# Performance work log

Hardware: AMD Instinct MI355X
Metric: run time of the kernel (lower is better)

The kernel has to match this reference:

```python
import jax, jax.numpy as jnp
import numpy as np

NHID = 512
T_K, T_Q, B = 256, 128, 8


def setup_inputs() -> dict:
    key = jax.random.key(0)
    k1, k2, k3, k4, k5 = jax.random.split(key, 5)
    query = jax.random.normal(k1, (T_Q, B, NHID), dtype=jnp.float32)
    c_key = jax.random.normal(k2, (T_K, B, NHID), dtype=jnp.float32)
    mask = jax.random.randint(k3, (T_K, B), 0, 2).astype(bool)
    # att_mlp params: Linear(2*nhid, nhid) -> Tanh -> Linear(nhid, 1)
    # stored as [in, out] so y = x @ W + b (torch Linear weight transposed)
    W1 = jax.random.normal(k4, (2 * NHID, NHID), dtype=jnp.float32) / np.sqrt(2 * NHID)
    b1 = jnp.zeros((NHID,), dtype=jnp.float32)
    W2 = jax.random.normal(k5, (NHID, 1), dtype=jnp.float32) / np.sqrt(NHID)
    b2 = jnp.zeros((1,), dtype=jnp.float32)
    return {"query": query, "c_key": c_key, "mask": mask,
            "W1": W1, "b1": b1, "W2": W2, "b2": b2}


def reference(query, c_key, mask, W1, b1, W2, b2):
    H = query.shape[-1]
    # cat([k_expand, q_expand], -1) @ W1 == k @ W1[:H] + q @ W1[H:]
    # (avoids materializing the [T_k, T_q, B, 2H] concat the torch code builds)
    k_proj = jnp.einsum('kbh,hd->kbd', c_key, W1[:H])   # [T_k, B, H]
    q_proj = jnp.einsum('qbh,hd->qbd', query, W1[H:])   # [T_q, B, H]
    h = jnp.tanh(k_proj[:, None, :, :] + q_proj[None, :, :, :] + b1)  # [T_k, T_q, B, H]
    att_score = jnp.einsum('kqbh,ho->kqb', h, W2) + b2[0]             # [T_k, T_q, B]
    att_score = jnp.where(mask[:, None, :], -jnp.inf, att_score)
    att_prob = jax.nn.softmax(att_score, axis=0)                      # softmax over keys
    # c_val defaults to c_key in the original forward
    ant_vec = jnp.einsum('kqb,kbh->qbh', att_prob, c_key)             # [T_q, B, H]
    return ant_vec, att_prob
```

## Files before the change

### kernel.cpp

```cpp
#include <hip/hip_runtime.h>
#include <math.h>

#define NHID 512
#define T_K  256
#define T_Q  128
#define BB   8

constexpr float C2L2E = 2.8853900817779268f;
constexpr float L2E   = 1.4426950408889634f;

__device__ __forceinline__ float fexp2(float x) { return __builtin_amdgcn_exp2f(x); }
__device__ __forceinline__ float frcp(float x)  { return __builtin_amdgcn_rcpf(x); }

typedef __attribute__((ext_vector_type(8))) short bf16x8;
typedef __attribute__((ext_vector_type(4))) float f32x4;

__device__ __forceinline__ unsigned short f2bf(float x) {
    unsigned u = __builtin_bit_cast(unsigned, x);
    unsigned r = (u + 0x7FFFu + ((u >> 16) & 1u)) >> 16;
    return (unsigned short)r;
}
__device__ __forceinline__ float bf2f(unsigned short h) {
    unsigned u = ((unsigned)h) << 16;
    return __builtin_bit_cast(float, u);
}
__device__ __forceinline__ unsigned packbf(float a, float b) {
    return (unsigned)f2bf(a) | ((unsigned)f2bf(b) << 16);
}

__global__ __launch_bounds__(256) void convert_kernel(
    const float* __restrict__ W1, const float* __restrict__ ckey,
    unsigned short* __restrict__ bt_hi, unsigned short* __restrict__ bt_lo,
    unsigned int* __restrict__ ckp)
{
    const int bid = blockIdx.x;
    const int t   = threadIdx.x;
    if (bid < 128) {
        const int kt = bid & 15;
        const int nt = bid >> 4;
        __shared__ float tile[64][65];
        const int r  = t >> 2;
        const int c0 = (t & 3) * 16;
        const float* src = W1 + (size_t)(kt * 64 + r) * 512 + nt * 64 + c0;
        #pragma unroll
        for (int j = 0; j < 4; ++j) {
            const float4 v = *(const float4*)&src[j * 4];
            tile[r][c0 + j * 4 + 0] = v.x; tile[r][c0 + j * 4 + 1] = v.y;
            tile[r][c0 + j * 4 + 2] = v.z; tile[r][c0 + j * 4 + 3] = v.w;
        }
        __syncthreads();
        const size_t dst = (size_t)((kt >> 3) * 512 + nt * 64 + r) * 512
                         + (size_t)((kt & 7) * 64 + c0);
        #pragma unroll
        for (int j4 = 0; j4 < 4; ++j4) {
            ushort4 h, l;
            #pragma unroll
            for (int e = 0; e < 4; ++e) {
                const float x = tile[c0 + j4 * 4 + e][r];
                const unsigned short hb = f2bf(x);
                ((unsigned short*)&h)[e] = hb;
                ((unsigned short*)&l)[e] = f2bf(x - bf2f(hb));
            }
            *(ushort4*)&bt_hi[dst + j4 * 4] = h;
            *(ushort4*)&bt_lo[dst + j4 * 4] = l;
        }
    } else {
        const int cb = bid - 128;
        const int b  = cb >> 5;
        const int kt = cb & 31;
        const int kloc = t >> 5;
        const int g    = t & 31;
        const int k = kt * 8 + kloc;
        const float* src = ckey + ((size_t)k * 8 + b) * 512 + g * 16;
        const float4 v0 = *(const float4*)&src[0];
        const float4 v1 = *(const float4*)&src[4];
        const float4 v2 = *(const float4*)&src[8];
        const float4 v3 = *(const float4*)&src[12];
        uint4 o0, o1;
        o0.x = packbf(v0.x, v0.y); o0.y = packbf(v0.z, v0.w);
        o0.z = packbf(v1.x, v1.y); o0.w = packbf(v1.z, v1.w);
        o1.x = packbf(v2.x, v2.y); o1.y = packbf(v2.z, v2.w);
        o1.z = packbf(v3.x, v3.y); o1.w = packbf(v3.z, v3.w);
        unsigned int* dst = ckp + ((size_t)b * 256 + k) * 256 + g * 8;
        *(uint4*)&dst[0] = o0;
        *(uint4*)&dst[4] = o1;
    }
}

__global__ __launch_bounds__(256) void proj_kernel(
    const float* __restrict__ qry, const float* __restrict__ ckey,
    const unsigned short* __restrict__ bt_hi, const unsigned short* __restrict__ bt_lo,
    const float* __restrict__ b1,
    uint2* __restrict__ ektq, float* __restrict__ eq)
{
    const int row0 = blockIdx.x * 32;
    const int col0 = blockIdx.y * 64;
    const bool isK = row0 < 2048;
    const int bhalf = isK ? 0 : 512;

    __shared__ __align__(16) unsigned short As_h[32 * 64];
    __shared__ __align__(16) unsigned short As_l[32 * 64];
    __shared__ __align__(16) unsigned short Bs_h[64 * 64];
    __shared__ __align__(16) unsigned short Bs_l[64 * 64];

    const int t    = threadIdx.x;
    const int wave = t >> 6;
    const int lane = t & 63;
    const int wm = (wave & 1) * 16;
    const int wn = (wave >> 1) * 32;

    f32x4 acc[2] = {};

    const int srA = t >> 3;
    const int scA = (t & 7) * 8;
    const float* gA = (isK ? ckey + (size_t)(row0 + srA) * 512
                           : qry  + (size_t)(row0 - 2048 + srA) * 512) + scA;
    const int swA = ((scA >> 3) ^ (srA & 7)) * 8;

    const int srB = t >> 2;
    const int scB = (t & 3) * 16;
    const unsigned short* gBh = bt_hi + (size_t)(bhalf + col0 + srB) * 512 + scB;
    const unsigned short* gBl = bt_lo + (size_t)(bhalf + col0 + srB) * 512 + scB;
    const int cB = scB >> 3;
    const int swB0 = ((cB + 0) ^ (srB & 7)) * 8;
    const int swB1 = ((cB + 1) ^ (srB & 7)) * 8;

    const int quad = lane >> 4, fr = lane & 15;

    float4 pa0 = *(const float4*)&gA[0];
    float4 pa1 = *(const float4*)&gA[4];
    uint4  pbh0 = *(const uint4*)&gBh[0], pbh1 = *(const uint4*)&gBh[8];
    uint4  pbl0 = *(const uint4*)&gBl[0], pbl1 = *(const uint4*)&gBl[8];

    for (int k0 = 0; k0 < 512; k0 += 64) {
        float fa[8];
        *(float4*)&fa[0] = pa0; *(float4*)&fa[4] = pa1;
        union { uint4 v; unsigned short s[8]; } h0, l0;
        #pragma unroll
        for (int e = 0; e < 8; ++e) {
            const unsigned short hb = f2bf(fa[e]);
            h0.s[e] = hb; l0.s[e] = f2bf(fa[e] - bf2f(hb));
        }
        __syncthreads();
        *(uint4*)&As_h[srA * 64 + swA] = h0.v;
        *(uint4*)&As_l[srA * 64 + swA] = l0.v;
        *(uint4*)&Bs_h[srB * 64 + swB0] = pbh0; *(uint4*)&Bs_h[srB * 64 + swB1] = pbh1;
        *(uint4*)&Bs_l[srB * 64 + swB0] = pbl0; *(uint4*)&Bs_l[srB * 64 + swB1] = pbl1;
        __syncthreads();

        if (k0 + 64 < 512) {
            pa0 = *(const float4*)&gA[k0 + 64];
            pa1 = *(const float4*)&gA[k0 + 68];
            pbh0 = *(const uint4*)&gBh[k0 + 64]; pbh1 = *(const uint4*)&gBh[k0 + 72];
            pbl0 = *(const uint4*)&gBl[k0 + 64]; pbl1 = *(const uint4*)&gBl[k0 + 72];
        }

        #pragma unroll
        for (int ks = 0; ks < 2; ++ks) {
            const int cchunk = ks * 4 + quad;
            const int m = wm + fr;
            const bf16x8 afh = *(const bf16x8*)&As_h[m * 64 + ((cchunk ^ (m & 7)) * 8)];
            const bf16x8 afl = *(const bf16x8*)&As_l[m * 64 + ((cchunk ^ (m & 7)) * 8)];
            bf16x8 bfh[2], bfl[2];
            #pragma unroll
            for (int nt = 0; nt < 2; ++nt) {
                const int n = wn + nt * 16 + fr;
                bfh[nt] = *(const bf16x8*)&Bs_h[n * 64 + ((cchunk ^ (n & 7)) * 8)];
                bfl[nt] = *(const bf16x8*)&Bs_l[n * 64 + ((cchunk ^ (n & 7)) * 8)];
            }
            #pragma unroll
            for (int nt = 0; nt < 2; ++nt) {
                acc[nt] = __builtin_amdgcn_mfma_f32_16x16x32_bf16(afh, bfh[nt], acc[nt], 0, 0, 0);
                acc[nt] = __builtin_amdgcn_mfma_f32_16x16x32_bf16(afh, bfl[nt], acc[nt], 0, 0, 0);
                acc[nt] = __builtin_amdgcn_mfma_f32_16x16x32_bf16(afl, bfh[nt], acc[nt], 0, 0, 0);
            }
        }
    }

    #pragma unroll
    for (int nt = 0; nt < 2; ++nt) {
        const int colg = col0 + wn + nt * 16 + fr;
        const float b1v = b1[colg];
        #pragma unroll
        for (int i = 0; i < 4; ++i) {
            const int rowg = row0 + wm + quad * 4 + i;
            const float v = acc[nt][i];
            if (isK) {
                const float e = fexp2((v + b1v) * C2L2E);
                const float ep = __shfl_xor(e, 1, 64);
                unsigned pk = ((fr & 1) == 0) ? packbf(e, ep) : packbf(ep, e);
                const unsigned pk2 = __shfl_xor(pk, 2, 64);
                if ((fr & 3) == 0) {
                    const int kidx = rowg >> 3;
                    const int bb   = rowg & 7;
                    const int hq   = colg >> 2;
                    ektq[((size_t)bb * 128 + hq) * 256 + kidx] = make_uint2(pk, pk2);
                }
            } else {
                eq[(size_t)(rowg - 2048) * 512 + colg] = fexp2(v * C2L2E);
            }
        }
    }
}

__global__ __launch_bounds__(512) void scoreav_kernel(
    const uint2* __restrict__ ektq, const float* __restrict__ eq,
    const float* __restrict__ W2, const float* __restrict__ b2,
    const int* __restrict__ mask, const unsigned int* __restrict__ ckp,
    float* __restrict__ prob_out, float* __restrict__ out_ant)
{
    const int t    = threadIdx.x;
    const int lane = t & 63;
    const int wave = __builtin_amdgcn_readfirstlane(t >> 6);
    const int kk   = t & 255;
    const int half = t >> 8;
    const int q0   = blockIdx.x * 2;
    const int b    = blockIdx.y;

    __shared__ float eq0s[512], eq1s[512], w2s[512];
    __shared__ float rp[2][512];
    __shared__ float ps[2][256];
    __shared__ float pacc[8][2][512];

    eq0s[t] = eq[((size_t)q0 * 8 + b) * 512 + t];
    eq1s[t] = eq[((size_t)(q0 + 1) * 8 + b) * 512 + t];
    w2s[t]  = W2[t];

    const float4 wA = *(const float4*)&W2[lane * 4];
    const float4 wB = *(const float4*)&W2[256 + lane * 4];
    float s2 = wA.x + wA.y + wA.z + wA.w + wB.x + wB.y + wB.z + wB.w;
    #pragma unroll
    for (int m = 32; m; m >>= 1) s2 += __shfl_xor(s2, m, 64);
    const float base = s2 + b2[0];
    __syncthreads();

    const uint2* __restrict__ ekb = ektq + (size_t)b * 128 * 256 + kk;
    float racc0 = 0.0f, racc1 = 0.0f;

    uint2 L[2][8];
    #pragma unroll
    for (int j = 0; j < 8; ++j)
        L[0][j] = ekb[(size_t)(half * 64 + j) * 256];

    for (int g = 0; g < 8; ++g) {
        const int cur = g & 1;
        if (g < 7) {
            #pragma unroll
            for (int j = 0; j < 8; ++j)
                L[cur ^ 1][j] = ekb[(size_t)(half * 64 + (g + 1) * 8 + j) * 256];
        }
        #pragma unroll
        for (int j = 0; j < 8; ++j) {
            const int h = (half * 64 + g * 8 + j) * 4;
            const float ek0 = __builtin_bit_cast(float, L[cur][j].x << 16);
            const float ek1 = __builtin_bit_cast(float, L[cur][j].x & 0xFFFF0000u);
            const float ek2 = __builtin_bit_cast(float, L[cur][j].y << 16);
            const float ek3 = __builtin_bit_cast(float, L[cur][j].y & 0xFFFF0000u);
            const float4 w  = *(const float4*)&w2s[h];
            const float4 e0 = *(const float4*)&eq0s[h];
            const float4 e1 = *(const float4*)&eq1s[h];
            {
                const float a0 = fmaf(ek0, e0.x, 1.0f);
                const float a1 = fmaf(ek1, e0.y, 1.0f);
                const float a2 = fmaf(ek2, e0.z, 1.0f);
                const float a3 = fmaf(ek3, e0.w, 1.0f);
                const float d01 = a0 * a1, d23 = a2 * a3;
                const float n01 = fmaf(w.x, a1, w.y * a0);
                const float n23 = fmaf(w.z, a3, w.w * a2);
                const float N = fmaf(n01, d23, n23 * d01);
                racc0 = fmaf(N, frcp(d01 * d23), racc0);
            }
            {
                const float a0 = fmaf(ek0, e1.x, 1.0f);
                const float a1 = fmaf(ek1, e1.y, 1.0f);
                const float a2 = fmaf(ek2, e1.z, 1.0f);
                const float a3 = fmaf(ek3, e1.w, 1.0f);
                const float d01 = a0 * a1, d23 = a2 * a3;
                const float n01 = fmaf(w.x, a1, w.y * a0);
                const float n23 = fmaf(w.z, a3, w.w * a2);
                const float N = fmaf(n01, d23, n23 * d01);
                racc1 = fmaf(N, frcp(d01 * d23), racc1);
            }
        }
    }
    rp[0][t] = racc0;
    rp[1][t] = racc1;
    __syncthreads();

    if (t < 256) {
        const int msk = mask[t * 8 + b];
        float s0 = base - 2.0f * (rp[0][t] + rp[0][t + 256]);
        float s1 = base - 2.0f * (rp[1][t] + rp[1][t + 256]);
        if (msk) { s0 = -INFINITY; s1 = -INFINITY; }
        ps[0][t] = s0;
        ps[1][t] = s1;
    }
    __syncthreads();

    if (wave < 2) {
        float4 sv = *(const float4*)&ps[wave][lane * 4];
        float m = fmaxf(fmaxf(sv.x, sv.y), fmaxf(sv.z, sv.w));
        #pragma unroll
        for (int d = 32; d; d >>= 1) m = fmaxf(m, __shfl_xor(m, d, 64));
        float4 pv;
        pv.x = fexp2((sv.x - m) * L2E);
        pv.y = fexp2((sv.y - m) * L2E);
        pv.z = fexp2((sv.z - m) * L2E);
        pv.w = fexp2((sv.w - m) * L2E);
        float sum = pv.x + pv.y + pv.z + pv.w;
        #pragma unroll
        for (int d = 32; d; d >>= 1) sum += __shfl_xor(sum, d, 64);
        const float inv = frcp(sum);
        pv.x *= inv; pv.y *= inv; pv.z *= inv; pv.w *= inv;
        *(float4*)&ps[wave][lane * 4] = pv;
        const int qb_idx = (q0 + wave) * 8 + b;
        const int kbase = lane * 4;
        prob_out[(size_t)(kbase + 0) * 1024 + qb_idx] = pv.x;
        prob_out[(size_t)(kbase + 1) * 1024 + qb_idx] = pv.y;
        prob_out[(size_t)(kbase + 2) * 1024 + qb_idx] = pv.z;
        prob_out[(size_t)(kbase + 3) * 1024 + qb_idx] = pv.w;
    }
    __syncthreads();

    {
        const int h0 = lane * 8;
        float4 aL0 = {}, aH0 = {}, aL1 = {}, aH1 = {};
        const int kstart = wave * 32;
        #pragma unroll 4
        for (int ki = 0; ki < 32; ++ki) {
            const int k = kstart + ki;
            const uint4 U = *(const uint4*)&ckp[((size_t)b * 256 + k) * 256 + lane * 4];
            float4 c0, c1;
            c0.x = __builtin_bit_cast(float, U.x << 16);
            c0.y = __builtin_bit_cast(float, U.x & 0xFFFF0000u);
            c0.z = __builtin_bit_cast(float, U.y << 16);
            c0.w = __builtin_bit_cast(float, U.y & 0xFFFF0000u);
            c1.x = __builtin_bit_cast(float, U.z << 16);
            c1.y = __builtin_bit_cast(float, U.z & 0xFFFF0000u);
            c1.z = __builtin_bit_cast(float, U.w << 16);
            c1.w = __builtin_bit_cast(float, U.w & 0xFFFF0000u);
            const float p0 = ps[0][k];
            const float p1 = ps[1][k];
            aL0.x = fmaf(p0, c0.x, aL0.x); aL0.y = fmaf(p0, c0.y, aL0.y);
            aL0.z = fmaf(p0, c0.z, aL0.z); aL0.w = fmaf(p0, c0.w, aL0.w);
            aH0.x = fmaf(p0, c1.x, aH0.x); aH0.y = fmaf(p0, c1.y, aH0.y);
            aH0.z = fmaf(p0, c1.z, aH0.z); aH0.w = fmaf(p0, c1.w, aH0.w);
            aL1.x = fmaf(p1, c0.x, aL1.x); aL1.y = fmaf(p1, c0.y, aL1.y);
            aL1.z = fmaf(p1, c0.z, aL1.z); aL1.w = fmaf(p1, c0.w, aL1.w);
            aH1.x = fmaf(p1, c1.x, aH1.x); aH1.y = fmaf(p1, c1.y, aH1.y);
            aH1.z = fmaf(p1, c1.z, aH1.z); aH1.w = fmaf(p1, c1.w, aH1.w);
        }
        *(float4*)&pacc[wave][0][h0 + 0] = aL0;
        *(float4*)&pacc[wave][0][h0 + 4] = aH0;
        *(float4*)&pacc[wave][1][h0 + 0] = aL1;
        *(float4*)&pacc[wave][1][h0 + 4] = aH1;
    }
    __syncthreads();

    {
        #pragma unroll
        for (int qi = 0; qi < 2; ++qi) {
            float s = 0.f;
            #pragma unroll
            for (int w = 0; w < 8; ++w) s += pacc[w][qi][t];
            out_ant[((size_t)(q0 + qi) * 8 + b) * 512 + t] = s;
        }
    }
}

extern "C" void kernel_launch(void* const* d_in, const int* in_sizes, int n_in,
                              void* d_out, int out_size, void* d_ws, size_t ws_size,
                              hipStream_t stream)
{
    const float* qry  = (const float*)d_in[0];
    const float* ckey = (const float*)d_in[1];
    const int*   mask = (const int*)d_in[2];
    const float* W1   = (const float*)d_in[3];
    const float* b1   = (const float*)d_in[4];
    const float* W2   = (const float*)d_in[5];
    const float* b2   = (const float*)d_in[6];

    float* out_ant  = (float*)d_out;
    float* out_prob = (float*)d_out + T_Q * BB * NHID;

    float* ws = (float*)d_ws;
    uint2* ws_ektq = (uint2*)ws;
    float* ws_eq  = ws + 524288;
    unsigned short* bt_hi = (unsigned short*)(ws + 1048576);
    unsigned short* bt_lo = (unsigned short*)(ws + 1310720);
    unsigned int* ws_ckp  = (unsigned int*)(ws + 1572864);

    convert_kernel<<<dim3(384), 256, 0, stream>>>(W1, ckey, bt_hi, bt_lo, ws_ckp);
    proj_kernel<<<dim3(96, 8), 256, 0, stream>>>(qry, ckey, bt_hi, bt_lo, b1, ws_ektq, ws_eq);
    scoreav_kernel<<<dim3(64, 8), 512, 0, stream>>>(ws_ektq, ws_eq, W2, b2, mask, ws_ckp,
                                                    out_prob, out_ant);
}
```

Measured before the change: 112.3 us.

## Split AV reduction across lanes with shuffles and add dual score accumulators

The attention-times-value stage is repartitioned: each wave now owns a 64-wide slice of the hidden dimension, and four lane groups each cover a quarter of the keys. The partial sums are combined with cross-lane shuffles instead of a 32 KB shared partial-accumulator buffer, a barrier and an extra LDS reduction pass, which also frees shared memory for occupancy. Separately, the score loop splits each running sum into two accumulators to shorten the dependent FMA chain. The trade-off is that global loads in the AV stage become narrower (8-byte loads, 128-byte runs per key row), and the shuffle reduction adds some extra instructions.

```diff
diff --git a/kernel.cpp b/kernel.cpp
--- a/kernel.cpp
+++ b/kernel.cpp
@@ -26,6 +26,12 @@
 }
 __device__ __forceinline__ unsigned packbf(float a, float b) {
     return (unsigned)f2bf(a) | ((unsigned)f2bf(b) << 16);
+}
+__device__ __forceinline__ float lo16(unsigned u) {
+    return __builtin_bit_cast(float, u << 16);
+}
+__device__ __forceinline__ float hi16(unsigned u) {
+    return __builtin_bit_cast(float, u & 0xFFFF0000u);
 }
 
 __global__ __launch_bounds__(256) void convert_kernel(
@@ -220,7 +226,6 @@
     __shared__ float eq0s[512], eq1s[512], w2s[512];
     __shared__ float rp[2][512];
     __shared__ float ps[2][256];
-    __shared__ float pacc[8][2][512];
 
     eq0s[t] = eq[((size_t)q0 * 8 + b) * 512 + t];
     eq1s[t] = eq[((size_t)(q0 + 1) * 8 + b) * 512 + t];
@@ -235,7 +240,7 @@
     __syncthreads();
 
     const uint2* __restrict__ ekb = ektq + (size_t)b * 128 * 256 + kk;
-    float racc0 = 0.0f, racc1 = 0.0f;
+    float r0a = 0.f, r0b = 0.f, r1a = 0.f, r1b = 0.f;
 
     uint2 L[2][8];
     #pragma unroll
@@ -252,10 +257,10 @@
         #pragma unroll
         for (int j = 0; j < 8; ++j) {
             const int h = (half * 64 + g * 8 + j) * 4;
-            const float ek0 = __builtin_bit_cast(float, L[cur][j].x << 16);
-            const float ek1 = __builtin_bit_cast(float, L[cur][j].x & 0xFFFF0000u);
-            const float ek2 = __builtin_bit_cast(float, L[cur][j].y << 16);
-            const float ek3 = __builtin_bit_cast(float, L[cur][j].y & 0xFFFF0000u);
+            const float ek0 = lo16(L[cur][j].x);
+            const float ek1 = hi16(L[cur][j].x);
+            const float ek2 = lo16(L[cur][j].y);
+            const float ek3 = hi16(L[cur][j].y);
             const float4 w  = *(const float4*)&w2s[h];
             const float4 e0 = *(const float4*)&eq0s[h];
             const float4 e1 = *(const float4*)&eq1s[h];
@@ -268,7 +273,8 @@
                 const float n01 = fmaf(w.x, a1, w.y * a0);
                 const float n23 = fmaf(w.z, a3, w.w * a2);
                 const float N = fmaf(n01, d23, n23 * d01);
-                racc0 = fmaf(N, frcp(d01 * d23), racc0);
+                if (j & 1) r0b = fmaf(N, frcp(d01 * d23), r0b);
+                else       r0a = fmaf(N, frcp(d01 * d23), r0a);
             }
             {
                 const float a0 = fmaf(ek0, e1.x, 1.0f);
@@ -279,12 +285,13 @@
                 const float n01 = fmaf(w.x, a1, w.y * a0);
                 const float n23 = fmaf(w.z, a3, w.w * a2);
                 const float N = fmaf(n01, d23, n23 * d01);
-                racc1 = fmaf(N, frcp(d01 * d23), racc1);
-            }
-        }
-    }
-    rp[0][t] = racc0;
-    rp[1][t] = racc1;
+                if (j & 1) r1b = fmaf(N, frcp(d01 * d23), r1b);
+                else       r1a = fmaf(N, frcp(d01 * d23), r1a);
+            }
+        }
+    }
+    rp[0][t] = r0a + r0b;
+    rp[1][t] = r1a + r1b;
     __syncthreads();
 
     if (t < 256) {
@@ -323,47 +330,36 @@
     __syncthreads();
 
     {
-        const int h0 = lane * 8;
-        float4 aL0 = {}, aH0 = {}, aL1 = {}, aH1 = {};
-        const int kstart = wave * 32;
-        #pragma unroll 4
-        for (int ki = 0; ki < 32; ++ki) {
-            const int k = kstart + ki;
-            const uint4 U = *(const uint4*)&ckp[((size_t)b * 256 + k) * 256 + lane * 4];
-            float4 c0, c1;
-            c0.x = __builtin_bit_cast(float, U.x << 16);
-            c0.y = __builtin_bit_cast(float, U.x & 0xFFFF0000u);
-            c0.z = __builtin_bit_cast(float, U.y << 16);
-            c0.w = __builtin_bit_cast(float, U.y & 0xFFFF0000u);
-            c1.x = __builtin_bit_cast(float, U.z << 16);
-            c1.y = __builtin_bit_cast(float, U.z & 0xFFFF0000u);
-            c1.z = __builtin_bit_cast(float, U.w << 16);
-            c1.w = __builtin_bit_cast(float, U.w & 0xFFFF0000u);
+        const int kq  = lane >> 4;
+        const int hq2 = lane & 15;
+        const int pbase = wave * 32 + hq2 * 2;
+        const unsigned int* __restrict__ ckb = ckp + (size_t)b * 256 * 256;
+        float4 a0 = {}, a1 = {};
+        #pragma unroll 8
+        for (int ki = 0; ki < 64; ++ki) {
+            const int k = ki * 4 + kq;
+            const uint2 U = *(const uint2*)&ckb[(size_t)k * 256 + pbase];
+            const float c0 = lo16(U.x), c1 = hi16(U.x);
+            const float c2 = lo16(U.y), c3 = hi16(U.y);
             const float p0 = ps[0][k];
             const float p1 = ps[1][k];
-            aL0.x = fmaf(p0, c0.x, aL0.x); aL0.y = fmaf(p0, c0.y, aL0.y);
-            aL0.z = fmaf(p0, c0.z, aL0.z); aL0.w = fmaf(p0, c0.w, aL0.w);
-            aH0.x = fmaf(p0, c1.x, aH0.x); aH0.y = fmaf(p0, c1.y, aH0.y);
-            aH0.z = fmaf(p0, c1.z, aH0.z); aH0.w = fmaf(p0, c1.w, aH0.w);
-            aL1.x = fmaf(p1, c0.x, aL1.x); aL1.y = fmaf(p1, c0.y, aL1.y);
-            aL1.z = fmaf(p1, c0.z, aL1.z); aL1.w = fmaf(p1, c0.w, aL1.w);
-            aH1.x = fmaf(p1, c1.x, aH1.x); aH1.y = fmaf(p1, c1.y, aH1.y);
-            aH1.z = fmaf(p1, c1.z, aH1.z); aH1.w = fmaf(p1, c1.w, aH1.w);
-        }
-        *(float4*)&pacc[wave][0][h0 + 0] = aL0;
-        *(float4*)&pacc[wave][0][h0 + 4] = aH0;
-        *(float4*)&pacc[wave][1][h0 + 0] = aL1;
-        *(float4*)&pacc[wave][1][h0 + 4] = aH1;
-    }
-    __syncthreads();
-
-    {
-        #pragma unroll
-        for (int qi = 0; qi < 2; ++qi) {
-            float s = 0.f;
-            #pragma unroll
-            for (int w = 0; w < 8; ++w) s += pacc[w][qi][t];
-            out_ant[((size_t)(q0 + qi) * 8 + b) * 512 + t] = s;
+            a0.x = fmaf(p0, c0, a0.x); a0.y = fmaf(p0, c1, a0.y);
+            a0.z = fmaf(p0, c2, a0.z); a0.w = fmaf(p0, c3, a0.w);
+            a1.x = fmaf(p1, c0, a1.x); a1.y = fmaf(p1, c1, a1.y);
+            a1.z = fmaf(p1, c2, a1.z); a1.w = fmaf(p1, c3, a1.w);
+        }
+        #pragma unroll
+        for (int d = 16; d <= 32; d <<= 1) {
+            a0.x += __shfl_xor(a0.x, d, 64); a0.y += __shfl_xor(a0.y, d, 64);
+            a0.z += __shfl_xor(a0.z, d, 64); a0.w += __shfl_xor(a0.w, d, 64);
+            a1.x += __shfl_xor(a1.x, d, 64); a1.y += __shfl_xor(a1.y, d, 64);
+            a1.z += __shfl_xor(a1.z, d, 64); a1.w += __shfl_xor(a1.w, d, 64);
+        }
+        if (lane < 32) {
+            const int qi = kq & 1;
+            const int h0 = wave * 64 + hq2 * 4;
+            const float4 outv = (qi == 0) ? a0 : a1;
+            *(float4*)&out_ant[((size_t)(q0 + qi) * 8 + b) * 512 + h0] = outv;
         }
     }
 }
```

After: 111.4 us. Within noise of the previous version (-0.8%).
